# Optimization experiments

Hardware: AMD Instinct MI355X
Metric: run time of the kernel (lower is better)

The kernel has to match this reference:

```python
import jax, jax.numpy as jnp
import numpy as np

L_SEQ = 32768
H_FEAT = 512
P_STATE = 256  # state_size // 2 (conj_sym)
LOG_DT_MIN, LOG_DT_MAX = np.log(1e-3), np.log(1e-1)


def setup_inputs() -> dict:
    key = jax.random.key(0)
    ks = jax.random.split(key, 7)
    input_sequence = jax.random.normal(ks[0], (L_SEQ, H_FEAT), dtype=jnp.float32)
    # eigenvalue real parts must be negative for stability (HiPPO-LegS-like)
    lambda_real = -jax.random.uniform(ks[1], (P_STATE,), minval=0.1, maxval=1.0, dtype=jnp.float32)
    lambda_imag = jax.random.normal(ks[2], (P_STATE,), dtype=jnp.float32) * float(np.pi)
    b = jax.random.normal(ks[3], (P_STATE, H_FEAT, 2), dtype=jnp.float32) / np.sqrt(H_FEAT)
    c = jax.random.normal(ks[4], (H_FEAT, P_STATE, 2), dtype=jnp.float32) / np.sqrt(P_STATE)
    d = jax.random.normal(ks[5], (H_FEAT,), dtype=jnp.float32)
    # log-timestep init in [log(1e-3), log(1e-1)] as in init_log_steps
    delta = (LOG_DT_MIN + jax.random.uniform(ks[6], (P_STATE, 1), dtype=jnp.float32)
             * (LOG_DT_MAX - LOG_DT_MIN))
    return {"input_sequence": input_sequence, "lambda_real": lambda_real,
            "lambda_imag": lambda_imag, "b": b, "c": c, "d": d, "delta": delta}


def _binop(e_i, e_j):
    A_i, b_i = e_i
    A_j, b_j = e_j
    return A_j * A_i, A_j * b_i + b_j


def reference(input_sequence, lambda_real, lambda_imag, b, c, d, delta):
    # assemble complex parameters (stored as real [..., 2])
    Lam = lambda_real + 1j * lambda_imag            # [P]
    B = b[..., 0] + 1j * b[..., 1]                  # [P, H]
    C = c[..., 0] + 1j * c[..., 1]                  # [H, P]
    step = jnp.exp(delta[:, 0])                     # step_rescale = 1.0
    # bilinear discretization
    BL = 1.0 / (1.0 - (step / 2.0) * Lam)
    Lam_bar = BL * (1.0 + (step / 2.0) * Lam)       # [P]
    B_bar = (BL * step)[:, None] * B                # [P, H]
    # input projection: Bu[l] = B_bar @ u[l]
    Bu = jnp.einsum('lh,ph->lp', input_sequence.astype(Lam_bar.dtype), B_bar)  # [L, P]
    L = input_sequence.shape[0]
    Lam_el = jnp.broadcast_to(Lam_bar, (L, Lam_bar.shape[0]))
    _, xs = jax.lax.associative_scan(_binop, (Lam_el, Bu))  # xs: [L, P] complex states
    # output projection (conj_sym => factor 2, real part)
    ys = 2.0 * jnp.einsum('lp,hp->lh', xs, C).real  # [L, H]
    return ys + d * input_sequence
```

## Files before the change

kernel.cpp:

```cpp
#include <hip/hip_runtime.h>
#include <cstddef>

#define L_SEQ 32768
#define H_FEAT 512
#define P_STATE 256
#define N2 512
#define CS 32
#define NCH (L_SEQ / CS)

typedef __bf16 bf16x8 __attribute__((ext_vector_type(8)));
typedef float f32x4 __attribute__((ext_vector_type(4)));

#define GLDS16(g, l) __builtin_amdgcn_global_load_lds( \
    (const __attribute__((address_space(1))) void*)(g), \
    (__attribute__((address_space(3))) void*)(l), 16, 0, 0)

#define SCHED_FENCE() __builtin_amdgcn_sched_barrier(0)

__device__ __forceinline__ unsigned bf_rne(float x) {
    unsigned u = __float_as_uint(x);
    return (u + 0x7fffu + ((u >> 16) & 1u)) >> 16;
}
__device__ __forceinline__ float bf_f(unsigned bits) {
    return __uint_as_float(bits << 16);
}
__device__ __forceinline__ float2 cmul(float2 a, float2 b) {
    return make_float2(fmaf(a.x, b.x, -a.y * b.y), fmaf(a.x, b.y, a.y * b.x));
}
__device__ __forceinline__ float2 cfma(float2 a, float2 b, float2 c) {
    return make_float2(fmaf(a.x, b.x, fmaf(-a.y, b.y, c.x)),
                       fmaf(a.x, b.y, fmaf(a.y, b.x, c.y)));
}

__global__ __launch_bounds__(256) void param_kernel(
    const float* __restrict__ lr, const float* __restrict__ li,
    const float* __restrict__ b,  const float* __restrict__ c,
    const float* __restrict__ delta,
    ushort* __restrict__ W_hi, ushort* __restrict__ W_lo,
    ushort* __restrict__ C2_hi, ushort* __restrict__ C2_lo,
    float2* __restrict__ Abar)
{
    int tid = blockIdx.x * blockDim.x + threadIdx.x;

    {
        int p = tid >> 9;
        int h = tid & 511;
        float step = expf(delta[p]);
        float zr = 0.5f * step * lr[p];
        float zi = 0.5f * step * li[p];
        float dr = 1.0f - zr, di = -zi;
        float den = dr * dr + di * di;
        float blr = dr / den, bli = -di / den;
        float bbr = blr * step, bbi = bli * step;
        float b0 = b[((size_t)(p * H_FEAT + h)) * 2 + 0];
        float b1 = b[((size_t)(p * H_FEAT + h)) * 2 + 1];
        float vr = bbr * b0 - bbi * b1;
        float vi = bbr * b1 + bbi * b0;
        unsigned hr = bf_rne(vr), hl = bf_rne(vr - bf_f(hr));
        unsigned ir = bf_rne(vi), il = bf_rne(vi - bf_f(ir));
        size_t o0 = (size_t)(2 * p) * H_FEAT + h;
        size_t o1 = (size_t)(2 * p + 1) * H_FEAT + h;
        W_hi[o0] = (ushort)hr; W_lo[o0] = (ushort)hl;
        W_hi[o1] = (ushort)ir; W_lo[o1] = (ushort)il;
    }

    {
        int h2 = tid >> 8;
        int p2 = tid & 255;
        float c0 =  2.0f * c[((size_t)(h2 * P_STATE + p2)) * 2 + 0];
        float c1 = -2.0f * c[((size_t)(h2 * P_STATE + p2)) * 2 + 1];
        unsigned h0 = bf_rne(c0), l0 = bf_rne(c0 - bf_f(h0));
        unsigned h1 = bf_rne(c1), l1 = bf_rne(c1 - bf_f(h1));
        size_t o0 = (size_t)h2 * N2 + 2 * p2;
        C2_hi[o0] = (ushort)h0;     C2_lo[o0] = (ushort)l0;
        C2_hi[o0 + 1] = (ushort)h1; C2_lo[o0 + 1] = (ushort)l1;
    }

    if (tid < P_STATE) {
        int p = tid;
        float step = expf(delta[p]);
        float zr = 0.5f * step * lr[p];
        float zi = 0.5f * step * li[p];
        float dr = 1.0f - zr, di = -zi;
        float den = dr * dr + di * di;
        float blr = dr / den, bli = -di / den;
        float nr = 1.0f + zr, ni = zi;
        Abar[p] = make_float2(blr * nr - bli * ni, blr * ni + bli * nr);
    }
}

__global__ __launch_bounds__(256, 2) void gemm1(
    const float* __restrict__ A,
    const ushort* __restrict__ Bhi, const ushort* __restrict__ Blo,
    float* __restrict__ C,
    const float2* __restrict__ Abar, float2* __restrict__ ends)
{
    __shared__ ushort sh[32768];
    ushort* As_hi = sh;
    ushort* As_lo = sh + 4096;
    ushort* Bs_hi = sh + 8192;
    ushort* Bs_lo = sh + 16384;
    float*  Cs    = (float*)sh;

    const int tid = threadIdx.x;
    const int ln = tid & 63, wv = tid >> 6;
    const int bm = blockIdx.y * 128, bn = blockIdx.x * 256;
    const int m = ln & 15, q = ln >> 4;
    const int wr = (wv >> 1) * 64, wc = (wv & 1) * 128;

    f32x4 acc[4][8] = {};

    for (int k0 = 0; k0 < 512; k0 += 32) {
#pragma unroll
        for (int s = 0; s < 8; s++) {
            int t = wv * 8 + s;
            int ch = t & 15;
            int row = ch * 16 + (ln >> 2);
            const ushort* src = (t < 16 ? Bhi : Blo)
                                + (size_t)(bn + row) * 512 + k0 + (ln & 3) * 8;
            ushort* dst = (t < 16 ? Bs_hi : Bs_lo) + ch * 512 + ln * 8;
            GLDS16(src, dst);
        }
#pragma unroll
        for (int r = 0; r < 4; r++) {
            int idx = tid + r * 256;
            int row = idx >> 3;
            int c4 = (idx & 7) << 2;
            const float4 v = *(const float4*)(A + (size_t)(bm + row) * 512 + k0 + c4);
            unsigned u0 = __float_as_uint(v.x), u1 = __float_as_uint(v.y);
            unsigned u2 = __float_as_uint(v.z), u3 = __float_as_uint(v.w);
            unsigned hi01 = (u0 >> 16) | (u1 & 0xffff0000u);
            unsigned hi23 = (u2 >> 16) | (u3 & 0xffff0000u);
            float d0 = v.x - __uint_as_float(u0 & 0xffff0000u);
            float d1 = v.y - __uint_as_float(u1 & 0xffff0000u);
            float d2 = v.z - __uint_as_float(u2 & 0xffff0000u);
            float d3 = v.w - __uint_as_float(u3 & 0xffff0000u);
            unsigned lo01 = (__float_as_uint(d0) >> 16) | (__float_as_uint(d1) & 0xffff0000u);
            unsigned lo23 = (__float_as_uint(d2) >> 16) | (__float_as_uint(d3) & 0xffff0000u);
            *(uint2*)(As_hi + row * 32 + c4) = make_uint2(hi01, hi23);
            *(uint2*)(As_lo + row * 32 + c4) = make_uint2(lo01, lo23);
        }
        __syncthreads();

        bf16x8 ah[4], al[4];
#pragma unroll
        for (int i = 0; i < 4; i++) {
            ah[i] = *(const bf16x8*)(As_hi + (wr + i * 16 + m) * 32 + q * 8);
            al[i] = *(const bf16x8*)(As_lo + (wr + i * 16 + m) * 32 + q * 8);
        }
#pragma unroll
        for (int j = 0; j < 8; j++) {
            bf16x8 bh = *(const bf16x8*)(Bs_hi + (wc + j * 16 + m) * 32 + q * 8);
            bf16x8 bl = *(const bf16x8*)(Bs_lo + (wc + j * 16 + m) * 32 + q * 8);
#pragma unroll
            for (int i = 0; i < 4; i++)
                acc[i][j] = __builtin_amdgcn_mfma_f32_16x16x32_bf16(ah[i], bh, acc[i][j], 0, 0, 0);
#pragma unroll
            for (int i = 0; i < 4; i++)
                acc[i][j] = __builtin_amdgcn_mfma_f32_16x16x32_bf16(al[i], bh, acc[i][j], 0, 0, 0);
#pragma unroll
            for (int i = 0; i < 4; i++)
                acc[i][j] = __builtin_amdgcn_mfma_f32_16x16x32_bf16(ah[i], bl, acc[i][j], 0, 0, 0);
        }
        __syncthreads();
    }

#pragma unroll
    for (int i = 0; i < 4; i++)
#pragma unroll
        for (int j = 0; j < 8; j++)
#pragma unroll
            for (int r = 0; r < 4; r++) {
                int row = bm + wr + i * 16 + q * 4 + r;
                int col = bn + wc + j * 16 + m;
                C[(size_t)row * 512 + col] = acc[i][j][r];
            }

    const int p_l = tid & 127;
    const int lc  = tid >> 7;
    const float2 Aop = Abar[(bn >> 1) + p_l];
#pragma unroll
    for (int h = 0; h < 2; h++) {
        if ((wv >> 1) == h) {
#pragma unroll
            for (int i = 0; i < 4; i++)
#pragma unroll
                for (int j = 0; j < 8; j++)
#pragma unroll
                    for (int r = 0; r < 4; r++)
                        Cs[(i * 16 + q * 4 + r) * 256 + wc + j * 16 + m] = acc[i][j][r];
        }
        __syncthreads();
        {
            float2 s = make_float2(0.f, 0.f);
#pragma unroll 8
            for (int i2 = 0; i2 < 32; i2++) {
                float2 u = *(const float2*)(Cs + (lc * 32 + i2) * 256 + 2 * p_l);
                s = cfma(Aop, s, u);
            }
            ends[(size_t)((bn >> 1) + p_l) * NCH + (bm >> 5) + h * 2 + lc] = s;
        }
        __syncthreads();
    }
}

__global__ __launch_bounds__(256, 2) void gemm2(
    const float* __restrict__ Bu,
    const ushort* __restrict__ Bhi, const ushort* __restrict__ Blo,
    float* __restrict__ Cout, const float* __restrict__ U,
    const float* __restrict__ dvec,
    const float2* __restrict__ Abar, const float2* __restrict__ carries)
{
    __shared__ ushort As_hi[128 * 32], As_lo[128 * 32];
    __shared__ ushort Bs_hi[256 * 32], Bs_lo[256 * 32];
    __shared__ float  Af32[128 * 32];
    const int tid = threadIdx.x;
    const int ln = tid & 63, wv = tid >> 6;
    const int bm = blockIdx.y * 128, bn = blockIdx.x * 256;
    const int m = ln & 15, q = ln >> 4;
    const int wr = (wv >> 1) * 64, wc = (wv & 1) * 128;

    const int pl = tid & 15, sg = (tid >> 4) & 3, chk = tid >> 6;

    f32x4 acc[4][8] = {};

    for (int k0 = 0; k0 < 512; k0 += 32) {
        const int pg = (k0 >> 1) + pl;
        float2 S = carries[(size_t)pg * NCH + (bm >> 5) + chk];
        float2 Aop2 = Abar[pg];
        SCHED_FENCE();
        float4 av[4];
#pragma unroll
        for (int r = 0; r < 4; r++) {
            int idx = tid + r * 256;
            int row = idx >> 3;
            int c4 = (idx & 7) << 2;
            av[r] = *(const float4*)(Bu + (size_t)(bm + row) * 512 + k0 + c4);
        }
        SCHED_FENCE();
#pragma unroll
        for (int s = 0; s < 8; s++) {
            int t = wv * 8 + s;
            int ch = t & 15;
            int row = ch * 16 + (ln >> 2);
            const ushort* src = (t < 16 ? Bhi : Blo)
                                + (size_t)(bn + row) * 512 + k0 + (ln & 3) * 8;
            ushort* dst = (t < 16 ? Bs_hi : Bs_lo) + ch * 512 + ln * 8;
            GLDS16(src, dst);
        }
        SCHED_FENCE();
#pragma unroll
        for (int r = 0; r < 4; r++) {
            int idx = tid + r * 256;
            int row = idx >> 3;
            int c4 = (idx & 7) << 2;
            *(float4*)(Af32 + row * 32 + c4) = av[r];
        }
        asm volatile("s_waitcnt vmcnt(8) lgkmcnt(0)" ::: "memory");
        SCHED_FENCE();
        __builtin_amdgcn_s_barrier();
        SCHED_FENCE();

        {
            const float2 A2 = cmul(Aop2, Aop2);
            const float2 A4 = cmul(A2, A2);
            const float2 A8 = cmul(A4, A4);
            const int rbase = chk * 32 + sg * 8;

            float2 lv[8];
            float2 s = make_float2(0.f, 0.f);
#pragma unroll
            for (int k = 0; k < 8; k++) {
                const float2 uvv = *(const float2*)(Af32 + (rbase + k) * 32 + 2 * pl);
                s = cfma(Aop2, s, uvv);
                lv[k] = s;
            }
            const float2 e0 = make_float2(__shfl(s.x, pl),      __shfl(s.y, pl));
            const float2 e1 = make_float2(__shfl(s.x, pl + 16), __shfl(s.y, pl + 16));
            const float2 e2 = make_float2(__shfl(s.x, pl + 32), __shfl(s.y, pl + 32));
            if (sg >= 1) S = cfma(A8, S, e0);
            if (sg >= 2) S = cfma(A8, S, e1);
            if (sg >= 3) S = cfma(A8, S, e2);
            float2 pw = Aop2;
#pragma unroll
            for (int k = 0; k < 8; k++) {
                const float sr = fmaf(pw.x, S.x, fmaf(-pw.y, S.y, lv[k].x));
                const float si = fmaf(pw.x, S.y, fmaf(pw.y, S.x, lv[k].y));
                unsigned hr  = bf_rne(sr);
                unsigned lr2 = __float_as_uint(sr - bf_f(hr)) >> 16;
                unsigned hi_ = bf_rne(si);
                unsigned li2 = __float_as_uint(si - bf_f(hi_)) >> 16;
                const int row = rbase + k;
                *(unsigned*)(As_hi + row * 32 + 2 * pl) = hr | (hi_ << 16);
                *(unsigned*)(As_lo + row * 32 + 2 * pl) = lr2 | (li2 << 16);
                pw = cmul(pw, Aop2);
            }
        }
        asm volatile("s_waitcnt vmcnt(0) lgkmcnt(0)" ::: "memory");
        SCHED_FENCE();
        __builtin_amdgcn_s_barrier();
        SCHED_FENCE();

        bf16x8 ah[4], al[4];
#pragma unroll
        for (int i = 0; i < 4; i++) {
            ah[i] = *(const bf16x8*)(As_hi + (wr + i * 16 + m) * 32 + q * 8);
            al[i] = *(const bf16x8*)(As_lo + (wr + i * 16 + m) * 32 + q * 8);
        }
#pragma unroll
        for (int j = 0; j < 8; j++) {
            bf16x8 bh = *(const bf16x8*)(Bs_hi + (wc + j * 16 + m) * 32 + q * 8);
            bf16x8 bl = *(const bf16x8*)(Bs_lo + (wc + j * 16 + m) * 32 + q * 8);
#pragma unroll
            for (int i = 0; i < 4; i++)
                acc[i][j] = __builtin_amdgcn_mfma_f32_16x16x32_bf16(ah[i], bh, acc[i][j], 0, 0, 0);
#pragma unroll
            for (int i = 0; i < 4; i++)
                acc[i][j] = __builtin_amdgcn_mfma_f32_16x16x32_bf16(al[i], bh, acc[i][j], 0, 0, 0);
#pragma unroll
            for (int i = 0; i < 4; i++)
                acc[i][j] = __builtin_amdgcn_mfma_f32_16x16x32_bf16(ah[i], bl, acc[i][j], 0, 0, 0);
        }
        __syncthreads();
    }

#pragma unroll
    for (int i = 0; i < 4; i++)
#pragma unroll
        for (int j = 0; j < 8; j++) {
            int col = bn + wc + j * 16 + m;
            float dv = dvec[col];
#pragma unroll
            for (int r = 0; r < 4; r++) {
                int row = bm + wr + i * 16 + q * 4 + r;
                Cout[(size_t)row * 512 + col] =
                    acc[i][j][r] + dv * U[(size_t)row * 512 + col];
            }
        }
}

__global__ __launch_bounds__(1024) void scan_pass2(
    const float2* __restrict__ ends, const float2* __restrict__ Abar,
    float2* __restrict__ carries)
{
    __shared__ float2 sA[NCH];
    __shared__ float2 sB[NCH];
    int p = blockIdx.x;
    int t = threadIdx.x;

    float2 a = Abar[p];
#pragma unroll
    for (int i = 0; i < 5; i++) {
        float nr = a.x * a.x - a.y * a.y;
        float ni = 2.f * a.x * a.y;
        a = make_float2(nr, ni);
    }
    float2 A = a;
    float2 bv = ends[(size_t)p * NCH + t];
    sA[t] = A; sB[t] = bv;
    __syncthreads();

    for (int off = 1; off < NCH; off <<= 1) {
        float2 pa, pb;
        bool act = (t >= off);
        if (act) { pa = sA[t - off]; pb = sB[t - off]; }
        __syncthreads();
        if (act) {
            float2 nA = make_float2(A.x * pa.x - A.y * pa.y,
                                    A.x * pa.y + A.y * pa.x);
            float2 nB = make_float2(fmaf(A.x, pb.x, fmaf(-A.y, pb.y, bv.x)),
                                    fmaf(A.x, pb.y, fmaf(A.y, pb.x, bv.y)));
            A = nA; bv = nB;
            sA[t] = A; sB[t] = bv;
        }
        __syncthreads();
    }

    float2 carry = (t == 0) ? make_float2(0.f, 0.f) : sB[t - 1];
    carries[(size_t)p * NCH + t] = carry;
}

extern "C" void kernel_launch(void* const* d_in, const int* in_sizes, int n_in,
                              void* d_out, int out_size, void* d_ws, size_t ws_size,
                              hipStream_t stream) {
    const float* u     = (const float*)d_in[0];
    const float* lr    = (const float*)d_in[1];
    const float* li    = (const float*)d_in[2];
    const float* b     = (const float*)d_in[3];
    const float* c     = (const float*)d_in[4];
    const float* dvec  = (const float*)d_in[5];
    const float* delta = (const float*)d_in[6];
    float* out = (float*)d_out;

    char* p = (char*)d_ws;
    float*  Bu      = (float*)p;   p += (size_t)L_SEQ * N2 * 4;
    float2* ends    = (float2*)p;  p += (size_t)P_STATE * NCH * 8;
    float2* carries = (float2*)p;  p += (size_t)P_STATE * NCH * 8;
    ushort* W_hi    = (ushort*)p;  p += (size_t)N2 * H_FEAT * 2;
    ushort* W_lo    = (ushort*)p;  p += (size_t)N2 * H_FEAT * 2;
    ushort* C2_hi   = (ushort*)p;  p += (size_t)H_FEAT * N2 * 2;
    ushort* C2_lo   = (ushort*)p;  p += (size_t)H_FEAT * N2 * 2;
    float2* Abar    = (float2*)p;  p += (size_t)P_STATE * 8;

    param_kernel<<<(P_STATE * H_FEAT) / 256, 256, 0, stream>>>(
        lr, li, b, c, delta, W_hi, W_lo, C2_hi, C2_lo, Abar);

    {
        dim3 grid(N2 / 256, L_SEQ / 128);
        gemm1<<<grid, 256, 0, stream>>>(u, W_hi, W_lo, Bu, Abar, ends);
    }

    scan_pass2<<<P_STATE, NCH, 0, stream>>>(ends, Abar, carries);

    {
        dim3 grid(H_FEAT / 256, L_SEQ / 128);
        gemm2<<<grid, 256, 0, stream>>>(Bu, C2_hi, C2_lo, out, u, dvec,
                                        Abar, carries);
    }
}
```

Measured before the change: 232.3 us.

## Split gemm2 into producer/consumer waves with double-buffered LDS

```diff
diff --git a/kernel.cpp b/kernel.cpp
--- a/kernel.cpp
+++ b/kernel.cpp
@@ -14,8 +14,6 @@
 #define GLDS16(g, l) __builtin_amdgcn_global_load_lds( \
     (const __attribute__((address_space(1))) void*)(g), \
     (__attribute__((address_space(3))) void*)(l), 16, 0, 0)
-
-#define SCHED_FENCE() __builtin_amdgcn_sched_barrier(0)
 
 __device__ __forceinline__ unsigned bf_rne(float x) {
     unsigned u = __float_as_uint(x);
@@ -204,139 +202,133 @@
     }
 }
 
-__global__ __launch_bounds__(256, 2) void gemm2(
+__global__ __launch_bounds__(512) void gemm2(
     const float* __restrict__ Bu,
     const ushort* __restrict__ Bhi, const ushort* __restrict__ Blo,
     float* __restrict__ Cout, const float* __restrict__ U,
     const float* __restrict__ dvec,
     const float2* __restrict__ Abar, const float2* __restrict__ carries)
 {
-    __shared__ ushort As_hi[128 * 32], As_lo[128 * 32];
-    __shared__ ushort Bs_hi[256 * 32], Bs_lo[256 * 32];
-    __shared__ float  Af32[128 * 32];
+    __shared__ ushort As_hi[2][128 * 32], As_lo[2][128 * 32];
+    __shared__ ushort Bs_hi[2][256 * 32], Bs_lo[2][256 * 32];
     const int tid = threadIdx.x;
+    const int bm = blockIdx.y * 128, bn = blockIdx.x * 256;
+    const bool producer = (tid >= 256);
+
     const int ln = tid & 63, wv = tid >> 6;
-    const int bm = blockIdx.y * 128, bn = blockIdx.x * 256;
     const int m = ln & 15, q = ln >> 4;
     const int wr = (wv >> 1) * 64, wc = (wv & 1) * 128;
 
-    const int pl = tid & 15, sg = (tid >> 4) & 3, chk = tid >> 6;
+    const int tid2 = tid & 255;
+    const int wv2 = tid2 >> 6, ln2 = tid2 & 63;
+    const int pl = tid2 & 15, sg = (tid2 >> 4) & 3, chk = tid2 >> 6;
 
     f32x4 acc[4][8] = {};
 
-    for (int k0 = 0; k0 < 512; k0 += 32) {
-        const int pg = (k0 >> 1) + pl;
-        float2 S = carries[(size_t)pg * NCH + (bm >> 5) + chk];
-        float2 Aop2 = Abar[pg];
-        SCHED_FENCE();
-        float4 av[4];
-#pragma unroll
-        for (int r = 0; r < 4; r++) {
-            int idx = tid + r * 256;
-            int row = idx >> 3;
-            int c4 = (idx & 7) << 2;
-            av[r] = *(const float4*)(Bu + (size_t)(bm + row) * 512 + k0 + c4);
-        }
-        SCHED_FENCE();
-#pragma unroll
-        for (int s = 0; s < 8; s++) {
-            int t = wv * 8 + s;
-            int ch = t & 15;
-            int row = ch * 16 + (ln >> 2);
-            const ushort* src = (t < 16 ? Bhi : Blo)
-                                + (size_t)(bn + row) * 512 + k0 + (ln & 3) * 8;
-            ushort* dst = (t < 16 ? Bs_hi : Bs_lo) + ch * 512 + ln * 8;
-            GLDS16(src, dst);
-        }
-        SCHED_FENCE();
-#pragma unroll
-        for (int r = 0; r < 4; r++) {
-            int idx = tid + r * 256;
-            int row = idx >> 3;
-            int c4 = (idx & 7) << 2;
-            *(float4*)(Af32 + row * 32 + c4) = av[r];
-        }
-        asm volatile("s_waitcnt vmcnt(8) lgkmcnt(0)" ::: "memory");
-        SCHED_FENCE();
-        __builtin_amdgcn_s_barrier();
-        SCHED_FENCE();
-
-        {
-            const float2 A2 = cmul(Aop2, Aop2);
-            const float2 A4 = cmul(A2, A2);
-            const float2 A8 = cmul(A4, A4);
-            const int rbase = chk * 32 + sg * 8;
-
-            float2 lv[8];
-            float2 s = make_float2(0.f, 0.f);
-#pragma unroll
-            for (int k = 0; k < 8; k++) {
-                const float2 uvv = *(const float2*)(Af32 + (rbase + k) * 32 + 2 * pl);
-                s = cfma(Aop2, s, uvv);
-                lv[k] = s;
+    for (int t = 0; t <= 16; ++t) {
+        if (producer) {
+            if (t < 16) {
+                const int k0 = t * 32;
+                const int buf = t & 1;
+                ushort* bsh = Bs_hi[buf];
+                ushort* bsl = Bs_lo[buf];
+#pragma unroll
+                for (int s = 0; s < 8; s++) {
+                    int tt = wv2 * 8 + s;
+                    int ch = tt & 15;
+                    int row = ch * 16 + (ln2 >> 2);
+                    const ushort* src = (tt < 16 ? Bhi : Blo)
+                                        + (size_t)(bn + row) * 512 + k0 + (ln2 & 3) * 8;
+                    ushort* dst = (tt < 16 ? bsh : bsl) + ch * 512 + ln2 * 8;
+                    GLDS16(src, dst);
+                }
+                const int pg = (k0 >> 1) + pl;
+                const float2 Aop2 = Abar[pg];
+                const float2 A2 = cmul(Aop2, Aop2);
+                const float2 A4 = cmul(A2, A2);
+                const float2 A8 = cmul(A4, A4);
+                const int rbase = chk * 32 + sg * 8;
+                float2 S = carries[(size_t)pg * NCH + (bm >> 5) + chk];
+
+                float2 lv[8];
+                float2 s = make_float2(0.f, 0.f);
+#pragma unroll
+                for (int k = 0; k < 8; k++) {
+                    const float2 uvv = *(const float2*)(
+                        Bu + (size_t)(bm + rbase + k) * 512 + k0 + 2 * pl);
+                    s = cfma(Aop2, s, uvv);
+                    lv[k] = s;
+                }
+                const float2 e0 = make_float2(__shfl(s.x, pl),      __shfl(s.y, pl));
+                const float2 e1 = make_float2(__shfl(s.x, pl + 16), __shfl(s.y, pl + 16));
+                const float2 e2 = make_float2(__shfl(s.x, pl + 32), __shfl(s.y, pl + 32));
+                if (sg >= 1) S = cfma(A8, S, e0);
+                if (sg >= 2) S = cfma(A8, S, e1);
+                if (sg >= 3) S = cfma(A8, S, e2);
+                ushort* ash = As_hi[buf];
+                ushort* asl = As_lo[buf];
+                float2 pw = Aop2;
+#pragma unroll
+                for (int k = 0; k < 8; k++) {
+                    const float sr = fmaf(pw.x, S.x, fmaf(-pw.y, S.y, lv[k].x));
+                    const float si = fmaf(pw.x, S.y, fmaf(pw.y, S.x, lv[k].y));
+                    unsigned hr  = bf_rne(sr);
+                    unsigned lr2 = __float_as_uint(sr - bf_f(hr)) >> 16;
+                    unsigned hi_ = bf_rne(si);
+                    unsigned li2 = __float_as_uint(si - bf_f(hi_)) >> 16;
+                    const int row = rbase + k;
+                    *(unsigned*)(ash + row * 32 + 2 * pl) = hr | (hi_ << 16);
+                    *(unsigned*)(asl + row * 32 + 2 * pl) = lr2 | (li2 << 16);
+                    pw = cmul(pw, Aop2);
+                }
             }
-            const float2 e0 = make_float2(__shfl(s.x, pl),      __shfl(s.y, pl));
-            const float2 e1 = make_float2(__shfl(s.x, pl + 16), __shfl(s.y, pl + 16));
-            const float2 e2 = make_float2(__shfl(s.x, pl + 32), __shfl(s.y, pl + 32));
-            if (sg >= 1) S = cfma(A8, S, e0);
-            if (sg >= 2) S = cfma(A8, S, e1);
-            if (sg >= 3) S = cfma(A8, S, e2);
-            float2 pw = Aop2;
-#pragma unroll
-            for (int k = 0; k < 8; k++) {
-                const float sr = fmaf(pw.x, S.x, fmaf(-pw.y, S.y, lv[k].x));
-                const float si = fmaf(pw.x, S.y, fmaf(pw.y, S.x, lv[k].y));
-                unsigned hr  = bf_rne(sr);
-                unsigned lr2 = __float_as_uint(sr - bf_f(hr)) >> 16;
-                unsigned hi_ = bf_rne(si);
-                unsigned li2 = __float_as_uint(si - bf_f(hi_)) >> 16;
-                const int row = rbase + k;
-                *(unsigned*)(As_hi + row * 32 + 2 * pl) = hr | (hi_ << 16);
-                *(unsigned*)(As_lo + row * 32 + 2 * pl) = lr2 | (li2 << 16);
-                pw = cmul(pw, Aop2);
+        } else {
+            if (t > 0) {
+                const int buf = (t - 1) & 1;
+                const ushort* ash = As_hi[buf];
+                const ushort* asl = As_lo[buf];
+                const ushort* bsh = Bs_hi[buf];
+                const ushort* bsl = Bs_lo[buf];
+                bf16x8 ah[4], al[4];
+#pragma unroll
+                for (int i = 0; i < 4; i++) {
+                    ah[i] = *(const bf16x8*)(ash + (wr + i * 16 + m) * 32 + q * 8);
+                    al[i] = *(const bf16x8*)(asl + (wr + i * 16 + m) * 32 + q * 8);
+                }
+#pragma unroll
+                for (int j = 0; j < 8; j++) {
+                    bf16x8 bh = *(const bf16x8*)(bsh + (wc + j * 16 + m) * 32 + q * 8);
+                    bf16x8 bl = *(const bf16x8*)(bsl + (wc + j * 16 + m) * 32 + q * 8);
+#pragma unroll
+                    for (int i = 0; i < 4; i++)
+                        acc[i][j] = __builtin_amdgcn_mfma_f32_16x16x32_bf16(ah[i], bh, acc[i][j], 0, 0, 0);
+#pragma unroll
+                    for (int i = 0; i < 4; i++)
+                        acc[i][j] = __builtin_amdgcn_mfma_f32_16x16x32_bf16(al[i], bh, acc[i][j], 0, 0, 0);
+#pragma unroll
+                    for (int i = 0; i < 4; i++)
+                        acc[i][j] = __builtin_amdgcn_mfma_f32_16x16x32_bf16(ah[i], bl, acc[i][j], 0, 0, 0);
+                }
             }
         }
-        asm volatile("s_waitcnt vmcnt(0) lgkmcnt(0)" ::: "memory");
-        SCHED_FENCE();
-        __builtin_amdgcn_s_barrier();
-        SCHED_FENCE();
-
-        bf16x8 ah[4], al[4];
-#pragma unroll
-        for (int i = 0; i < 4; i++) {
-            ah[i] = *(const bf16x8*)(As_hi + (wr + i * 16 + m) * 32 + q * 8);
-            al[i] = *(const bf16x8*)(As_lo + (wr + i * 16 + m) * 32 + q * 8);
-        }
-#pragma unroll
-        for (int j = 0; j < 8; j++) {
-            bf16x8 bh = *(const bf16x8*)(Bs_hi + (wc + j * 16 + m) * 32 + q * 8);
-            bf16x8 bl = *(const bf16x8*)(Bs_lo + (wc + j * 16 + m) * 32 + q * 8);
-#pragma unroll
-            for (int i = 0; i < 4; i++)
-                acc[i][j] = __builtin_amdgcn_mfma_f32_16x16x32_bf16(ah[i], bh, acc[i][j], 0, 0, 0);
-#pragma unroll
-            for (int i = 0; i < 4; i++)
-                acc[i][j] = __builtin_amdgcn_mfma_f32_16x16x32_bf16(al[i], bh, acc[i][j], 0, 0, 0);
-#pragma unroll
-            for (int i = 0; i < 4; i++)
-                acc[i][j] = __builtin_amdgcn_mfma_f32_16x16x32_bf16(ah[i], bl, acc[i][j], 0, 0, 0);
-        }
-        __syncthreads();
-    }
-
-#pragma unroll
-    for (int i = 0; i < 4; i++)
-#pragma unroll
-        for (int j = 0; j < 8; j++) {
-            int col = bn + wc + j * 16 + m;
-            float dv = dvec[col];
-#pragma unroll
-            for (int r = 0; r < 4; r++) {
-                int row = bm + wr + i * 16 + q * 4 + r;
-                Cout[(size_t)row * 512 + col] =
-                    acc[i][j][r] + dv * U[(size_t)row * 512 + col];
+        __syncthreads();
+    }
+
+    if (!producer) {
+#pragma unroll
+        for (int i = 0; i < 4; i++)
+#pragma unroll
+            for (int j = 0; j < 8; j++) {
+                int col = bn + wc + j * 16 + m;
+                float dv = dvec[col];
+#pragma unroll
+                for (int r = 0; r < 4; r++) {
+                    int row = bm + wr + i * 16 + q * 4 + r;
+                    Cout[(size_t)row * 512 + col] =
+                        acc[i][j][r] + dv * U[(size_t)row * 512 + col];
+                }
             }
-        }
+    }
 }
 
 __global__ __launch_bounds__(1024) void scan_pass2(
@@ -414,7 +406,7 @@
 
     {
         dim3 grid(H_FEAT / 256, L_SEQ / 128);
-        gemm2<<<grid, 256, 0, stream>>>(Bu, C2_hi, C2_lo, out, u, dvec,
+        gemm2<<<grid, 512, 0, stream>>>(Bu, C2_hi, C2_lo, out, u, dvec,
                                         Abar, carries);
     }
 }
```

Result: slower. 241.5 us (+4.0%).
